# Kernel optimization log

Hardware: AMD Instinct MI355X
Metric: run time of the kernel (lower is better)

The kernel has to match this reference:

```python
import jax, jax.numpy as jnp
import numpy as np

B, IN, H0, H1, OUT = 4096, 1024, 4096, 4096, 1024
QMAX = 127.0


def setup_inputs() -> dict:
    key = jax.random.key(0)
    k0, k1, k2, k3 = jax.random.split(key, 4)
    x = jax.random.normal(k0, (B, IN), dtype=jnp.float32)
    # Linear weights hold already-quantized integer values (module casts .int())
    W0 = jax.random.randint(k1, (H0, IN + 1), -127, 128).astype(jnp.int32)
    W1 = jax.random.randint(k2, (H1, H0 + 1), -127, 128).astype(jnp.int32)
    W2 = jax.random.randint(k3, (OUT, H1 + 1), -127, 128).astype(jnp.int32)
    return {
        "x": x,
        "a_in0": jnp.float32(4.0), "a_w0": jnp.float32(0.05),
        "a_in2": jnp.float32(50.0), "a_w2": jnp.float32(0.05),
        "a_in4": jnp.float32(50.0), "a_w4": jnp.float32(0.05),
        "W0": W0, "W1": W1, "W2": W2,
    }


def _quant(x, amax):
    # clamp(round(x * 127/amax), -127, 127) -> int32
    return jnp.clip(jnp.round(x * (QMAX / amax)), -QMAX, QMAX).astype(jnp.int32)


def _qlinear(x, W, a_in, a_w):
    q = _quant(x, a_in)                                   # [B, K] int32
    ones = jnp.ones((q.shape[0], 1), dtype=jnp.int32)     # folded bias column
    q = jnp.concatenate([q, ones], axis=1)                # [B, K+1]
    acc = q @ W.T                                         # int32 GEMM [B, N]
    return acc.astype(jnp.float32) * (a_w * a_in / (QMAX * QMAX))


def reference(x, a_in0, a_w0, a_in2, a_w2, a_in4, a_w4, W0, W1, W2):
    x = x.reshape(x.shape[0], -1)
    x = _qlinear(x, W0, a_in0, a_w0)
    x = jax.nn.relu(x)
    x = _qlinear(x, W1, a_in2, a_w2)
    x = jax.nn.relu(x)
    x = _qlinear(x, W2, a_in4, a_w4)
    return x
```

## Files before the change

### kernel.cpp

```cpp
#include <hip/hip_runtime.h>

#define QMAX 127.0f

typedef int v4i __attribute__((ext_vector_type(4)));

__device__ __forceinline__ void gload_lds16(const void* g, void* l) {
  __builtin_amdgcn_global_load_lds(
      (const __attribute__((address_space(1))) void*)g,
      (__attribute__((address_space(3))) void*)l, 16, 0, 0);
}

__device__ __forceinline__ void pack_body(const int* __restrict__ W,
                                          signed char* __restrict__ W8,
                                          int* __restrict__ bias,
                                          unsigned lblk, int kshift) {
  unsigned t = lblk * 256u + threadIdx.x;
  unsigned row = t >> kshift;
  unsigned j = t & ((1u << kshift) - 1u);
  unsigned K = 4u << kshift;
  size_t srcBase = (size_t)row * (size_t)(K + 1) + (size_t)j * 4;
  int c0 = W[srcBase + 0], c1 = W[srcBase + 1], c2 = W[srcBase + 2], c3 = W[srcBase + 3];
  unsigned packed = (unsigned)(c0 & 0xff) | ((unsigned)(c1 & 0xff) << 8) |
                    ((unsigned)(c2 & 0xff) << 16) | ((unsigned)(c3 & 0xff) << 24);
  reinterpret_cast<unsigned*>(W8)[t] = packed;
  if (j == 0) bias[row] = W[(size_t)row * (K + 1) + K];
}

__global__ void prep_kernel(const float* __restrict__ x,
                            signed char* __restrict__ qa0,
                            const float* __restrict__ pAin,
                            const int* __restrict__ W0, signed char* __restrict__ W0p, int* __restrict__ b0,
                            const int* __restrict__ W1, signed char* __restrict__ W1p, int* __restrict__ b1,
                            const int* __restrict__ W2, signed char* __restrict__ W2p, int* __restrict__ b2) {
  unsigned blk = blockIdx.x;
  if (blk < 4096u) {
    pack_body(W0, W0p, b0, blk, 8);
  } else if (blk < 20480u) {
    pack_body(W1, W1p, b1, blk - 4096u, 10);
  } else if (blk < 24576u) {
    pack_body(W2, W2p, b2, blk - 20480u, 10);
  } else {
    unsigned t = (blk - 24576u) * 256u + threadIdx.x;
    float s = QMAX / pAin[0];
    float4 v = reinterpret_cast<const float4*>(x)[t];
    int q0 = (int)fminf(fmaxf(rintf(v.x * s), -QMAX), QMAX);
    int q1 = (int)fminf(fmaxf(rintf(v.y * s), -QMAX), QMAX);
    int q2 = (int)fminf(fmaxf(rintf(v.z * s), -QMAX), QMAX);
    int q3 = (int)fminf(fmaxf(rintf(v.w * s), -QMAX), QMAX);
    unsigned packed = (unsigned)(q0 & 0xff) | ((unsigned)(q1 & 0xff) << 8) |
                      ((unsigned)(q2 & 0xff) << 16) | ((unsigned)(q3 & 0xff) << 24);
    reinterpret_cast<unsigned*>(qa0)[t] = packed;
  }
}


#define FENCE() asm volatile("" ::: "memory")
#define BARRIER()                      \
  do {                                 \
    FENCE();                           \
    __builtin_amdgcn_s_barrier();      \
    FENCE();                           \
  } while (0)
#define LGK(n) asm volatile("s_waitcnt lgkmcnt(" #n ")" ::: "memory")
#define VMC0() asm volatile("s_waitcnt vmcnt(0)" ::: "memory")

#define STAGE_A(bf, h, t)                                                     \
  do {                                                                        \
    const signed char* _g = gA + (size_t)((h) * 128) * K + (size_t)(t) * 128; \
    signed char* _l = ldsA + (bf) * 32768 + (h) * 16384 + ldsThr;             \
    gload_lds16(_g, _l);                                                      \
    gload_lds16(_g + (size_t)8 * K, _l + 1024);                               \
  } while (0)

#define STAGE_B(bf, h, t)                                                     \
  do {                                                                        \
    const signed char* _g = gB + (size_t)((h) * 128) * K + (size_t)(t) * 128; \
    signed char* _l = ldsB + (bf) * 32768 + (h) * 16384 + ldsThr;             \
    gload_lds16(_g, _l);                                                      \
    gload_lds16(_g + (size_t)8 * K, _l + 1024);                               \
  } while (0)

#define STAGE_T(bf, t)                                                        \
  do {                                                                        \
    STAGE_A(bf, 0, t); STAGE_A(bf, 1, t);                                     \
    STAGE_B(bf, 0, t); STAGE_B(bf, 1, t);                                     \
  } while (0)

#define LDA8(bf, kk, dst)                                                     \
  do {                                                                        \
    _Pragma("unroll") for (int m = 0; m < 8; ++m) {                           \
      int row = wm * 128 + m * 16 + l15;                                      \
      int off = ((kk) * 64 + hi * 16) ^ ((l15 & 7) << 4);                     \
      dst[m] = *(const v4i*)(ldsA + (bf) * 32768 + row * 128 + off);          \
    }                                                                         \
  } while (0)

#define LDB4(bf, kk)                                                          \
  do {                                                                        \
    _Pragma("unroll") for (int n = 0; n < 4; ++n) {                           \
      int row = wn * 64 + n * 16 + l15;                                       \
      int off = ((kk) * 64 + hi * 16) ^ ((l15 & 7) << 4);                     \
      bK[n] = *(const v4i*)(ldsB + (bf) * 32768 + row * 128 + off);           \
    }                                                                         \
  } while (0)

#define MFMA32(aset)                                                          \
  do {                                                                        \
    __builtin_amdgcn_s_setprio(1);                                            \
    _Pragma("unroll") for (int m = 0; m < 8; ++m)                             \
    _Pragma("unroll") for (int n = 0; n < 4; ++n)                             \
      acc[m][n] = __builtin_amdgcn_mfma_i32_16x16x64_i8(                      \
          aset[m], bK[n], acc[m][n], 0, 0, 0);                                \
    __builtin_amdgcn_s_setprio(0);                                            \
  } while (0)

__global__ __launch_bounds__(512, 2)
void qgemm256_kernel(const signed char* __restrict__ A,
                     const signed char* __restrict__ Bw,
                     const int* __restrict__ bias,
                     signed char* __restrict__ O,
                     int N, int K, int nbn,
                     const float* __restrict__ pAin,
                     const float* __restrict__ pAw,
                     const float* __restrict__ pAnext) {
  extern __shared__ signed char lds[];
  signed char* ldsA = lds;
  signed char* ldsB = lds + 65536;

  const int nwg = gridDim.x, bid = blockIdx.x, per = nwg >> 3;
  const int swz = (bid & 7) * per + (bid >> 3);
  const int brow = swz / nbn, bcol = swz - brow * nbn;
  const int browBase = brow << 8, bcolBase = bcol << 8;

  const int tid = threadIdx.x;
  const int lane = tid & 63, l15 = lane & 15, hi = lane >> 4;
  const int wid = tid >> 6, wm = wid >> 2, wn = wid & 3;

  const int rloc = (wid << 4) + (lane >> 3);
  const int csrc = (lane & 7) ^ ((lane >> 3) & 7);
  const signed char* gA = A + (size_t)(browBase + rloc) * K + csrc * 16;
  const signed char* gB = Bw + (size_t)(bcolBase + rloc) * K + csrc * 16;
  const int ldsThr = (wid << 11) + lane * 16;

  v4i acc[8][4] = {};
  v4i aK0[8], aK1[8], bK[4];

  const int nk = K >> 7, niter = nk >> 1, nkm = nk - 1;

  STAGE_T(0, 0);
  VMC0();
  BARRIER();
  LDA8(0, 0, aK0);

#pragma unroll 1
  for (int i = 0; i < niter; ++i) {
    const int tO = 2 * i + 1;
    const int tE = (2 * i + 2) & nkm;
    LGK(8);
    BARRIER();
    STAGE_T(1, tO);
    LDB4(0, 0); FENCE(); LDA8(0, 1, aK1);
    LGK(8);
    MFMA32(aK0);
    VMC0();
    BARRIER();
    LDB4(0, 1); FENCE(); LDA8(1, 0, aK0);
    LGK(8);
    MFMA32(aK1);
    LGK(8);
    BARRIER();
    STAGE_T(0, tE);
    LDB4(1, 0); FENCE(); LDA8(1, 1, aK1);
    LGK(8);
    MFMA32(aK0);
    VMC0();
    BARRIER();
    LDB4(1, 1); FENCE(); LDA8(0, 0, aK0);
    LGK(8);
    MFMA32(aK1);
  }

  VMC0();

  const float sDeq = (pAw[0] * pAin[0]) / (QMAX * QMAX);
  const float sQ = QMAX / pAnext[0];
#pragma unroll
  for (int nf = 0; nf < 4; ++nf) {
    const int gcol = bcolBase + wn * 64 + nf * 16 + l15;
    const int bv = bias[gcol];
#pragma unroll
    for (int mf = 0; mf < 8; ++mf) {
      const int gr = browBase + wm * 128 + mf * 16 + (hi << 2);
#pragma unroll
      for (int r = 0; r < 4; ++r) {
        float f = (float)(acc[mf][nf][r] + bv) * sDeq;
        f = fmaxf(f, 0.0f);
        float qf = fminf(fmaxf(rintf(f * sQ), -QMAX), QMAX);
        O[(size_t)(gr + r) * N + gcol] = (signed char)(int)qf;
      }
    }
  }
}

#define STG128(bf, t)                                                         \
  do {                                                                        \
    _Pragma("unroll") for (int ii = 0; ii < 4; ++ii) {                        \
      int c = ii * 256 + tid;                                                 \
      int r = c >> 3;                                                         \
      int osrc = ((c & 7) << 4) ^ ((r & 7) << 4);                             \
      gload_lds16(A + (size_t)(browBase + r) * K + ((t) * 128 + osrc),        \
                  ldsA + (bf) * 16384 + c * 16);                              \
      gload_lds16(Bw + (size_t)(bcolBase + r) * K + ((t) * 128 + osrc),       \
                  ldsB + (bf) * 16384 + c * 16);                              \
    }                                                                         \
  } while (0)

#define LDA4_128(bf, kk, dst)                                                 \
  do {                                                                        \
    _Pragma("unroll") for (int m = 0; m < 4; ++m) {                           \
      int row = wr + m * 16 + l15;                                            \
      int off = ((kk) * 64 + hi * 16) ^ ((l15 & 7) << 4);                     \
      dst[m] = *(const v4i*)(ldsA + (bf) * 16384 + row * 128 + off);          \
    }                                                                         \
  } while (0)

#define LDB4_128(bf, kk)                                                      \
  do {                                                                        \
    _Pragma("unroll") for (int n = 0; n < 4; ++n) {                           \
      int row = wc + n * 16 + l15;                                            \
      int off = ((kk) * 64 + hi * 16) ^ ((l15 & 7) << 4);                     \
      bK[n] = *(const v4i*)(ldsB + (bf) * 16384 + row * 128 + off);           \
    }                                                                         \
  } while (0)

#define MFMA16(aset)                                                          \
  do {                                                                        \
    __builtin_amdgcn_s_setprio(1);                                            \
    _Pragma("unroll") for (int m = 0; m < 4; ++m)                             \
    _Pragma("unroll") for (int n = 0; n < 4; ++n)                             \
      acc[m][n] = __builtin_amdgcn_mfma_i32_16x16x64_i8(                      \
          aset[m], bK[n], acc[m][n], 0, 0, 0);                                \
    __builtin_amdgcn_s_setprio(0);                                            \
  } while (0)

__global__ __launch_bounds__(256)
void qgemm_kernel(const signed char* __restrict__ A,
                  const signed char* __restrict__ Bw,
                  const int* __restrict__ bias,
                  float* __restrict__ O,
                  int N, int K, int nbn,
                  const float* __restrict__ pAin,
                  const float* __restrict__ pAw) {
  __shared__ signed char slds[65536];
  signed char* ldsA = slds;
  signed char* ldsB = slds + 32768;

  const int nwg = gridDim.x, bid = blockIdx.x, per = nwg >> 3;
  const int swz = (bid & 7) * per + (bid >> 3);
  const int brow = swz / nbn, bcol = swz - brow * nbn;
  const int browBase = brow << 7, bcolBase = bcol << 7;

  const int tid = threadIdx.x;
  const int lane = tid & 63, l15 = lane & 15, hi = lane >> 4;
  const int wid = tid >> 6;
  const int wr = (wid >> 1) << 6, wc = (wid & 1) << 6;

  v4i acc[4][4] = {};
  v4i aK0[4], aK1[4], bK[4];

  const int nk = K >> 7, niter = nk >> 1, nkm = nk - 1;

  STG128(0, 0);
  VMC0();
  BARRIER();
  LDA4_128(0, 0, aK0);

#pragma unroll 1
  for (int i = 0; i < niter; ++i) {
    const int tO = 2 * i + 1;
    const int tE = (2 * i + 2) & nkm;
    LGK(4);
    BARRIER();
    STG128(1, tO);
    LDB4_128(0, 0); FENCE(); LDA4_128(0, 1, aK1);
    LGK(4);
    MFMA16(aK0);
    VMC0();
    BARRIER();
    LDB4_128(0, 1); FENCE(); LDA4_128(1, 0, aK0);
    LGK(4);
    MFMA16(aK1);
    LGK(4);
    BARRIER();
    STG128(0, tE);
    LDB4_128(1, 0); FENCE(); LDA4_128(1, 1, aK1);
    LGK(4);
    MFMA16(aK0);
    VMC0();
    BARRIER();
    LDB4_128(1, 1); FENCE(); LDA4_128(0, 0, aK0);
    LGK(4);
    MFMA16(aK1);
  }

  VMC0();

  const float sDeq = (pAw[0] * pAin[0]) / (QMAX * QMAX);
#pragma unroll
  for (int n = 0; n < 4; ++n) {
    int gcol = bcolBase + wc + n * 16 + l15;
    int bv = bias[gcol];
#pragma unroll
    for (int m = 0; m < 4; ++m) {
      int growb = browBase + wr + m * 16 + (hi << 2);
#pragma unroll
      for (int r = 0; r < 4; ++r) {
        O[(size_t)(growb + r) * N + gcol] = (float)(acc[m][n][r] + bv) * sDeq;
      }
    }
  }
}

extern "C" void kernel_launch(void* const* d_in, const int* in_sizes, int n_in,
                              void* d_out, int out_size, void* d_ws, size_t ws_size,
                              hipStream_t stream) {
  const float* x     = (const float*)d_in[0];
  const float* a_in0 = (const float*)d_in[1];
  const float* a_w0  = (const float*)d_in[2];
  const float* a_in2 = (const float*)d_in[3];
  const float* a_w2  = (const float*)d_in[4];
  const float* a_in4 = (const float*)d_in[5];
  const float* a_w4  = (const float*)d_in[6];
  const int*   W0    = (const int*)d_in[7];
  const int*   W1    = (const int*)d_in[8];
  const int*   W2    = (const int*)d_in[9];
  float* out = (float*)d_out;

  constexpr int B = 4096, IN = 1024, H0 = 4096, H1 = 4096, OUTN = 1024;

  char* ws = (char*)d_ws;
  size_t off = 0;
  auto alloc = [&](size_t sz) {
    char* p = ws + off;
    off += (sz + 255) & ~(size_t)255;
    return p;
  };
  signed char* qa0 = (signed char*)alloc((size_t)B * IN);
  signed char* qa1 = (signed char*)alloc((size_t)B * H0);
  signed char* qa2 = (signed char*)alloc((size_t)B * H1);
  signed char* W0p = (signed char*)alloc((size_t)H0 * IN);
  signed char* W1p = (signed char*)alloc((size_t)H1 * H0);
  signed char* W2p = (signed char*)alloc((size_t)OUTN * H1);
  int* b0 = (int*)alloc((size_t)H0 * 4);
  int* b1 = (int*)alloc((size_t)H1 * 4);
  int* b2 = (int*)alloc((size_t)OUTN * 4);

  hipFuncSetAttribute((const void*)qgemm256_kernel,
                      hipFuncAttributeMaxDynamicSharedMemorySize, 131072);

  prep_kernel<<<28672, 256, 0, stream>>>(x, qa0, a_in0,
                                         W0, W0p, b0,
                                         W1, W1p, b1,
                                         W2, W2p, b2);

  qgemm256_kernel<<<(B / 256) * (H0 / 256), 512, 131072, stream>>>(
      qa0, W0p, b0, qa1, H0, IN, H0 / 256, a_in0, a_w0, a_in2);

  qgemm256_kernel<<<(B / 256) * (H1 / 256), 512, 131072, stream>>>(
      qa1, W1p, b1, qa2, H1, H0, H1 / 256, a_in2, a_w2, a_in4);

  qgemm_kernel<<<(B / 128) * (OUTN / 128), 256, 0, stream>>>(
      qa2, W2p, b2, out, OUTN, H1, OUTN / 128, a_in4, a_w4);
}
```

Baseline: 139.9 us.

## Load A operand directly from global into registers, stage only B in LDS

The 256x256 int8 GEMM kernel no longer stages the activation (A) tile through LDS. Each wave now loads its A fragments straight from global memory into registers, while only the weight tile B still goes through LDS. Waits move from lgkmcnt-based counting to vmcnt-based counting, with fewer barriers per iteration and LDS halved to 64KB. The aim is to cut LDS traffic and barrier synchronisation and free LDS for occupancy. The cost is uncoalesced global loads of A, since waves sharing rows (wn 0..3) each fetch the same A data, which relies on L2 and cache hits and leaves more global latency exposed.

```diff
diff --git a/kernel.cpp b/kernel.cpp
--- a/kernel.cpp
+++ b/kernel.cpp
@@ -61,16 +61,8 @@
     __builtin_amdgcn_s_barrier();      \
     FENCE();                           \
   } while (0)
-#define LGK(n) asm volatile("s_waitcnt lgkmcnt(" #n ")" ::: "memory")
-#define VMC0() asm volatile("s_waitcnt vmcnt(0)" ::: "memory")
-
-#define STAGE_A(bf, h, t)                                                     \
-  do {                                                                        \
-    const signed char* _g = gA + (size_t)((h) * 128) * K + (size_t)(t) * 128; \
-    signed char* _l = ldsA + (bf) * 32768 + (h) * 16384 + ldsThr;             \
-    gload_lds16(_g, _l);                                                      \
-    gload_lds16(_g + (size_t)8 * K, _l + 1024);                               \
-  } while (0)
+#define LGK0() asm volatile("s_waitcnt lgkmcnt(0)" ::: "memory")
+#define VMC(n) asm volatile("s_waitcnt vmcnt(" #n ")" ::: "memory")
 
 #define STAGE_B(bf, h, t)                                                     \
   do {                                                                        \
@@ -80,19 +72,11 @@
     gload_lds16(_g + (size_t)8 * K, _l + 1024);                               \
   } while (0)
 
-#define STAGE_T(bf, t)                                                        \
-  do {                                                                        \
-    STAGE_A(bf, 0, t); STAGE_A(bf, 1, t);                                     \
-    STAGE_B(bf, 0, t); STAGE_B(bf, 1, t);                                     \
-  } while (0)
-
-#define LDA8(bf, kk, dst)                                                     \
-  do {                                                                        \
-    _Pragma("unroll") for (int m = 0; m < 8; ++m) {                           \
-      int row = wm * 128 + m * 16 + l15;                                      \
-      int off = ((kk) * 64 + hi * 16) ^ ((l15 & 7) << 4);                     \
-      dst[m] = *(const v4i*)(ldsA + (bf) * 32768 + row * 128 + off);          \
-    }                                                                         \
+#define GLA8(t, kk, dst)                                                      \
+  do {                                                                        \
+    _Pragma("unroll") for (int m = 0; m < 8; ++m)                             \
+      dst[m] = *(const v4i*)(gAf + (size_t)(m * 16) * K +                     \
+                             (size_t)(t) * 128 + (kk) * 64);                  \
   } while (0)
 
 #define LDB4(bf, kk)                                                          \
@@ -124,8 +108,7 @@
                      const float* __restrict__ pAw,
                      const float* __restrict__ pAnext) {
   extern __shared__ signed char lds[];
-  signed char* ldsA = lds;
-  signed char* ldsB = lds + 65536;
+  signed char* ldsB = lds;
 
   const int nwg = gridDim.x, bid = blockIdx.x, per = nwg >> 3;
   const int swz = (bid & 7) * per + (bid >> 3);
@@ -138,49 +121,54 @@
 
   const int rloc = (wid << 4) + (lane >> 3);
   const int csrc = (lane & 7) ^ ((lane >> 3) & 7);
-  const signed char* gA = A + (size_t)(browBase + rloc) * K + csrc * 16;
   const signed char* gB = Bw + (size_t)(bcolBase + rloc) * K + csrc * 16;
   const int ldsThr = (wid << 11) + lane * 16;
 
+  const signed char* gAf =
+      A + (size_t)(browBase + wm * 128 + l15) * K + hi * 16;
+
   v4i acc[8][4] = {};
   v4i aK0[8], aK1[8], bK[4];
 
   const int nk = K >> 7, niter = nk >> 1, nkm = nk - 1;
 
-  STAGE_T(0, 0);
-  VMC0();
+  STAGE_B(0, 0, 0); STAGE_B(0, 1, 0);
+  GLA8(0, 0, aK0);
+  VMC(8);
   BARRIER();
-  LDA8(0, 0, aK0);
 
 #pragma unroll 1
   for (int i = 0; i < niter; ++i) {
+    const int tC = 2 * i;
     const int tO = 2 * i + 1;
-    const int tE = (2 * i + 2) & nkm;
-    LGK(8);
-    BARRIER();
-    STAGE_T(1, tO);
-    LDB4(0, 0); FENCE(); LDA8(0, 1, aK1);
-    LGK(8);
+    const int tN = (2 * i + 2) & nkm;
+    STAGE_B(1, 0, tO); STAGE_B(1, 1, tO);
+    GLA8(tC, 1, aK1);
+    LDB4(0, 0);
+    VMC(12);
+    LGK0();
     MFMA32(aK0);
-    VMC0();
-    BARRIER();
-    LDB4(0, 1); FENCE(); LDA8(1, 0, aK0);
-    LGK(8);
+    GLA8(tO, 0, aK0);
+    LDB4(0, 1);
+    VMC(8);
+    LGK0();
     MFMA32(aK1);
-    LGK(8);
-    BARRIER();
-    STAGE_T(0, tE);
-    LDB4(1, 0); FENCE(); LDA8(1, 1, aK1);
-    LGK(8);
+    BARRIER();
+    STAGE_B(0, 0, tN); STAGE_B(0, 1, tN);
+    GLA8(tO, 1, aK1);
+    LDB4(1, 0);
+    VMC(12);
+    LGK0();
     MFMA32(aK0);
-    VMC0();
-    BARRIER();
-    LDB4(1, 1); FENCE(); LDA8(0, 0, aK0);
-    LGK(8);
+    GLA8(tN, 0, aK0);
+    LDB4(1, 1);
+    VMC(8);
+    LGK0();
     MFMA32(aK1);
-  }
-
-  VMC0();
+    BARRIER();
+  }
+
+  VMC(0);
 
   const float sDeq = (pAw[0] * pAin[0]) / (QMAX * QMAX);
   const float sQ = QMAX / pAnext[0];
@@ -201,6 +189,8 @@
     }
   }
 }
+
+#define LGK(n) asm volatile("s_waitcnt lgkmcnt(" #n ")" ::: "memory")
 
 #define STG128(bf, t)                                                         \
   do {                                                                        \
@@ -271,7 +261,7 @@
   const int nk = K >> 7, niter = nk >> 1, nkm = nk - 1;
 
   STG128(0, 0);
-  VMC0();
+  VMC(0);
   BARRIER();
   LDA4_128(0, 0, aK0);
 
@@ -285,7 +275,7 @@
     LDB4_128(0, 0); FENCE(); LDA4_128(0, 1, aK1);
     LGK(4);
     MFMA16(aK0);
-    VMC0();
+    VMC(0);
     BARRIER();
     LDB4_128(0, 1); FENCE(); LDA4_128(1, 0, aK0);
     LGK(4);
@@ -296,14 +286,14 @@
     LDB4_128(1, 0); FENCE(); LDA4_128(1, 1, aK1);
     LGK(4);
     MFMA16(aK0);
-    VMC0();
+    VMC(0);
     BARRIER();
     LDB4_128(1, 1); FENCE(); LDA4_128(0, 0, aK0);
     LGK(4);
     MFMA16(aK1);
   }
 
-  VMC0();
+  VMC(0);
 
   const float sDeq = (pAw[0] * pAin[0]) / (QMAX * QMAX);
 #pragma unroll
@@ -356,17 +346,17 @@
   int* b2 = (int*)alloc((size_t)OUTN * 4);
 
   hipFuncSetAttribute((const void*)qgemm256_kernel,
-                      hipFuncAttributeMaxDynamicSharedMemorySize, 131072);
+                      hipFuncAttributeMaxDynamicSharedMemorySize, 65536);
 
   prep_kernel<<<28672, 256, 0, stream>>>(x, qa0, a_in0,
                                          W0, W0p, b0,
                                          W1, W1p, b1,
                                          W2, W2p, b2);
 
-  qgemm256_kernel<<<(B / 256) * (H0 / 256), 512, 131072, stream>>>(
+  qgemm256_kernel<<<(B / 256) * (H0 / 256), 512, 65536, stream>>>(
       qa0, W0p, b0, qa1, H0, IN, H0 / 256, a_in0, a_w0, a_in2);
 
-  qgemm256_kernel<<<(B / 256) * (H1 / 256), 512, 131072, stream>>>(
+  qgemm256_kernel<<<(B / 256) * (H1 / 256), 512, 65536, stream>>>(
       qa1, W1p, b1, qa2, H1, H0, H1 / 256, a_in2, a_w2, a_in4);
 
   qgemm_kernel<<<(B / 128) * (OUTN / 128), 256, 0, stream>>>(
```

Result: slower. 227.8 us (+62.8%).

## Restructure 256-tile int8 GEMM mainloop into fine-grained staged quarter pipeline

Applied to the files above, without the earlier changes.

Replaces the two-phase double-buffered mainloop of the 256x256 int8 GEMM with an eight-phase schedule. Each phase loads a quarter of the A fragments from LDS, issues one half-tile global-to-LDS stage, and runs 16 MFMAs, with barriers between phases. The prologue prefetches most of the next k-tile and waits with a partial vmcnt, so global loads overlap compute more finely and fewer A registers are live at once. This adds many more barriers per iteration and relies on fragile waitcnt accounting. The swizzle expressions are rewritten to use row&7, which is equivalent to the old l15&7 because row offsets are multiples of 16.

```diff
diff --git a/kernel.cpp b/kernel.cpp
--- a/kernel.cpp
+++ b/kernel.cpp
@@ -61,7 +61,9 @@
     __builtin_amdgcn_s_barrier();      \
     FENCE();                           \
   } while (0)
+#define LGK0() asm volatile("s_waitcnt lgkmcnt(0)" ::: "memory")
 #define LGK(n) asm volatile("s_waitcnt lgkmcnt(" #n ")" ::: "memory")
+#define VMC6() asm volatile("s_waitcnt vmcnt(6)" ::: "memory")
 #define VMC0() asm volatile("s_waitcnt vmcnt(0)" ::: "memory")
 
 #define STAGE_A(bf, h, t)                                                     \
@@ -80,37 +82,31 @@
     gload_lds16(_g + (size_t)8 * K, _l + 1024);                               \
   } while (0)
 
-#define STAGE_T(bf, t)                                                        \
-  do {                                                                        \
-    STAGE_A(bf, 0, t); STAGE_A(bf, 1, t);                                     \
-    STAGE_B(bf, 0, t); STAGE_B(bf, 1, t);                                     \
-  } while (0)
-
-#define LDA8(bf, kk, dst)                                                     \
-  do {                                                                        \
-    _Pragma("unroll") for (int m = 0; m < 8; ++m) {                           \
-      int row = wm * 128 + m * 16 + l15;                                      \
-      int off = ((kk) * 64 + hi * 16) ^ ((l15 & 7) << 4);                     \
+#define LDAQ(bf, qm, kk, dst)                                                 \
+  do {                                                                        \
+    _Pragma("unroll") for (int m = 0; m < 4; ++m) {                           \
+      int row = wm * 128 + (qm) * 64 + m * 16 + l15;                          \
+      int off = ((kk) * 64 + hi * 16) ^ ((row & 7) << 4);                     \
       dst[m] = *(const v4i*)(ldsA + (bf) * 32768 + row * 128 + off);          \
     }                                                                         \
   } while (0)
 
-#define LDB4(bf, kk)                                                          \
+#define LDBH(bf, kk)                                                          \
   do {                                                                        \
     _Pragma("unroll") for (int n = 0; n < 4; ++n) {                           \
       int row = wn * 64 + n * 16 + l15;                                       \
-      int off = ((kk) * 64 + hi * 16) ^ ((l15 & 7) << 4);                     \
-      bK[n] = *(const v4i*)(ldsB + (bf) * 32768 + row * 128 + off);           \
-    }                                                                         \
-  } while (0)
-
-#define MFMA32(aset)                                                          \
+      int off = ((kk) * 64 + hi * 16) ^ ((row & 7) << 4);                     \
+      bR[n][kk] = *(const v4i*)(ldsB + (bf) * 32768 + row * 128 + off);       \
+    }                                                                         \
+  } while (0)
+
+#define MFMAQK(qm, kk, asrc)                                                  \
   do {                                                                        \
     __builtin_amdgcn_s_setprio(1);                                            \
-    _Pragma("unroll") for (int m = 0; m < 8; ++m)                             \
+    _Pragma("unroll") for (int m = 0; m < 4; ++m)                             \
     _Pragma("unroll") for (int n = 0; n < 4; ++n)                             \
-      acc[m][n] = __builtin_amdgcn_mfma_i32_16x16x64_i8(                      \
-          aset[m], bK[n], acc[m][n], 0, 0, 0);                                \
+      acc[(qm) * 4 + m][n] = __builtin_amdgcn_mfma_i32_16x16x64_i8(           \
+          asrc[m], bR[n][kk], acc[(qm) * 4 + m][n], 0, 0, 0);                 \
     __builtin_amdgcn_s_setprio(0);                                            \
   } while (0)
 
@@ -143,41 +139,65 @@
   const int ldsThr = (wid << 11) + lane * 16;
 
   v4i acc[8][4] = {};
-  v4i aK0[8], aK1[8], bK[4];
+  v4i bR[4][2];
 
   const int nk = K >> 7, niter = nk >> 1, nkm = nk - 1;
 
-  STAGE_T(0, 0);
-  VMC0();
+  STAGE_B(0, 0, 0); STAGE_B(0, 1, 0); STAGE_A(0, 0, 0); STAGE_A(0, 1, 0);
+  STAGE_B(1, 0, 1); STAGE_B(1, 1, 1); STAGE_A(1, 0, 1);
+  VMC6();
   BARRIER();
-  LDA8(0, 0, aK0);
 
 #pragma unroll 1
   for (int i = 0; i < niter; ++i) {
-    const int tO = 2 * i + 1;
+    const int t1 = 2 * i + 1;
     const int tE = (2 * i + 2) & nkm;
-    LGK(8);
-    BARRIER();
-    STAGE_T(1, tO);
-    LDB4(0, 0); FENCE(); LDA8(0, 1, aK1);
-    LGK(8);
-    MFMA32(aK0);
-    VMC0();
-    BARRIER();
-    LDB4(0, 1); FENCE(); LDA8(1, 0, aK0);
-    LGK(8);
-    MFMA32(aK1);
-    LGK(8);
-    BARRIER();
-    STAGE_T(0, tE);
-    LDB4(1, 0); FENCE(); LDA8(1, 1, aK1);
-    LGK(8);
-    MFMA32(aK0);
-    VMC0();
-    BARRIER();
-    LDB4(1, 1); FENCE(); LDA8(0, 0, aK0);
-    LGK(8);
-    MFMA32(aK1);
+    const int tO = (2 * i + 3) & nkm;
+    v4i a00[4], a01[4], a10[4], a11[4];
+    LDAQ(0, 0, 0, a00); LDBH(0, 0); LDAQ(0, 0, 1, a01); LDBH(0, 1);
+    STAGE_A(1, 1, t1);
+    BARRIER();
+    MFMAQK(0, 0, a00);
+    LGK0();
+    BARRIER();
+    LDAQ(0, 1, 0, a10);
+    STAGE_B(0, 0, tE);
+    BARRIER();
+    MFMAQK(0, 1, a01);
+    BARRIER();
+    LDAQ(0, 1, 1, a11);
+    STAGE_B(0, 1, tE);
+    BARRIER();
+    MFMAQK(1, 0, a10);
+    LGK0();
+    BARRIER();
+    STAGE_A(0, 0, tE);
+    VMC6();
+    BARRIER();
+    MFMAQK(1, 1, a11);
+    BARRIER();
+    LDAQ(1, 0, 0, a00); LDBH(1, 0); LDAQ(1, 0, 1, a01); LDBH(1, 1);
+    STAGE_A(0, 1, tE);
+    BARRIER();
+    MFMAQK(0, 0, a00);
+    LGK0();
+    BARRIER();
+    LDAQ(1, 1, 0, a10);
+    STAGE_B(1, 0, tO);
+    BARRIER();
+    MFMAQK(0, 1, a01);
+    BARRIER();
+    LDAQ(1, 1, 1, a11);
+    STAGE_B(1, 1, tO);
+    BARRIER();
+    MFMAQK(1, 0, a10);
+    LGK0();
+    BARRIER();
+    STAGE_A(1, 0, tO);
+    VMC6();
+    BARRIER();
+    MFMAQK(1, 1, a11);
+    BARRIER();
   }
 
   VMC0();
@@ -207,10 +227,10 @@
     _Pragma("unroll") for (int ii = 0; ii < 4; ++ii) {                        \
       int c = ii * 256 + tid;                                                 \
       int r = c >> 3;                                                         \
-      int osrc = ((c & 7) << 4) ^ ((r & 7) << 4);                             \
-      gload_lds16(A + (size_t)(browBase + r) * K + ((t) * 128 + osrc),        \
+      int osrc2 = ((c & 7) << 4) ^ ((r & 7) << 4);                            \
+      gload_lds16(A + (size_t)(browBase + r) * K + ((t) * 128 + osrc2),       \
                   ldsA + (bf) * 16384 + c * 16);                              \
-      gload_lds16(Bw + (size_t)(bcolBase + r) * K + ((t) * 128 + osrc),       \
+      gload_lds16(Bw + (size_t)(bcolBase + r) * K + ((t) * 128 + osrc2),      \
                   ldsB + (bf) * 16384 + c * 16);                              \
     }                                                                         \
   } while (0)
@@ -219,7 +239,7 @@
   do {                                                                        \
     _Pragma("unroll") for (int m = 0; m < 4; ++m) {                           \
       int row = wr + m * 16 + l15;                                            \
-      int off = ((kk) * 64 + hi * 16) ^ ((l15 & 7) << 4);                     \
+      int off = ((kk) * 64 + hi * 16) ^ ((row & 7) << 4);                     \
       dst[m] = *(const v4i*)(ldsA + (bf) * 16384 + row * 128 + off);          \
     }                                                                         \
   } while (0)
@@ -228,7 +248,7 @@
   do {                                                                        \
     _Pragma("unroll") for (int n = 0; n < 4; ++n) {                           \
       int row = wc + n * 16 + l15;                                            \
-      int off = ((kk) * 64 + hi * 16) ^ ((l15 & 7) << 4);                     \
+      int off = ((kk) * 64 + hi * 16) ^ ((row & 7) << 4);                     \
       bK[n] = *(const v4i*)(ldsB + (bf) * 16384 + row * 128 + off);           \
     }                                                                         \
   } while (0)
```

New measurement: 132.4 us. -5.4%, faster.
